# Optimization experiments

Measured on AMD Instinct MI355X. Metric: run time of the kernel, lower is better.

Reference implementation:

```python
import jax, jax.numpy as jnp
import numpy as np

B, N, D = 4, 4096, 1024
H, HD = 16, 64            # num_heads, head_dim (dim // num_heads)
K_ANCHOR = 256
SCALE = 1.0 / np.sqrt(float(HD))


def setup_inputs() -> dict:
    key = jax.random.key(0)
    ks = jax.random.split(key, 12)
    init = lambda k, shape, fan_in: jax.random.normal(k, shape, jnp.float32) * (1.0 / np.sqrt(fan_in))
    return {
        "x": jax.random.normal(ks[0], (B, N, D), jnp.float32),
        "Wq": init(ks[1], (D, H * HD), D), "bq": jnp.zeros((H * HD,), jnp.float32),
        "Wk": init(ks[2], (D, H * HD), D), "bk": jnp.zeros((H * HD,), jnp.float32),
        "Wv": init(ks[3], (D, H * HD), D), "bv": jnp.zeros((H * HD,), jnp.float32),
        "Wqt": init(ks[4], (D, D), D),     "bqt": jnp.zeros((D,), jnp.float32),
        "Wo": init(ks[5], (H * HD, D), H * HD), "bo": jnp.zeros((D,), jnp.float32),
        "num_anchor_tokens": K_ANCHOR,
    }


def _split_heads(t):
    # [B, S, H*HD] -> [B, H, S, HD]
    b, s, _ = t.shape
    return t.reshape(b, s, H, HD).transpose(0, 2, 1, 3)


def reference(x, Wq, bq, Wk, bk, Wv, bv, Wqt, bqt, Wo, bo, num_anchor_tokens):
    K = num_anchor_tokens  # static python int
    anchors = x[:, :K]     # [B, K, D]
    queries = x[:, K:]     # [B, N-K, D]

    q_a = anchors @ Wq + bq           # [B, K, H*HD]
    k_a = anchors @ Wk + bk           # [B, K, H*HD]
    v_a = anchors @ Wv + bv           # [B, K, H*HD]
    q_q = queries @ Wqt + bqt         # [B, N-K, H*HD] (dim == H*HD)

    q = _split_heads(jnp.concatenate([q_a, q_q], axis=1))  # [B, H, N, HD]
    k = _split_heads(k_a)                                  # [B, H, K, HD]
    v = _split_heads(v_a)                                  # [B, H, K, HD]

    scores = jnp.einsum("bhnd,bhkd->bhnk", q, k) * SCALE   # [B, H, N, K]
    weights = jax.nn.softmax(scores, axis=-1)
    ctx = jnp.einsum("bhnk,bhkd->bhnd", weights, v)        # [B, H, N, HD]
    ctx = ctx.transpose(0, 2, 1, 3).reshape(x.shape[0], x.shape[1], H * HD)
    return ctx @ Wo + bo               # [B, N, D]
```

## Files before the change

### kernel.cpp

```cpp
#include <hip/hip_runtime.h>
#include <stdint.h>
#include <stddef.h>


typedef _Float16 v8hf __attribute__((ext_vector_type(8)));
typedef _Float16 h4   __attribute__((ext_vector_type(4)));
typedef float    f32x4 __attribute__((ext_vector_type(4)));
typedef uint32_t u32x4 __attribute__((ext_vector_type(4)));

#define ATT_SCALE 0.125f
#define LOG2E     1.44269504088896340736f
#define QK_CE     (ATT_SCALE * LOG2E)

__device__ __forceinline__ void async16(const void* g, void* l) {
  __builtin_amdgcn_global_load_lds(
      (const __attribute__((address_space(1))) void*)g,
      (__attribute__((address_space(3))) void*)l,
      16, 0, 0);
}

__device__ __forceinline__ uint32_t pk_h2(float a, float b) {
  auto w = __builtin_amdgcn_cvt_pkrtz(a, b);
  return __builtin_bit_cast(uint32_t, w);
}

__global__ __launch_bounds__(256) void cvt_kernel(const float* __restrict__ src,
                                                  _Float16* __restrict__ dst, int n) {
  int i = (blockIdx.x * 256 + threadIdx.x) * 4;
  if (i + 3 < n) {
    float4 v = *(const float4*)(src + i);
    h4 o; o[0] = (_Float16)v.x; o[1] = (_Float16)v.y; o[2] = (_Float16)v.z; o[3] = (_Float16)v.w;
    *(h4*)(dst + i) = o;
  }
}

struct TPArgs { const float* src[5]; _Float16* dst[5]; };

__global__ __launch_bounds__(256) void transpose5_k(TPArgs a) {
  __shared__ _Float16 t[32][33];
  const int z = blockIdx.z;
  const float* __restrict__ src = a.src[z];
  _Float16* __restrict__ dst = a.dst[z];
  const int bx = blockIdx.x * 32, by = blockIdx.y * 32;
  const int x = threadIdx.x;
  for (int yy = threadIdx.y; yy < 32; yy += 8)
    t[yy][x] = (_Float16)src[(size_t)(by + yy) * 1024 + bx + x];
  __syncthreads();
  for (int yy = threadIdx.y; yy < 32; yy += 8)
    dst[(size_t)(bx + yy) * 1024 + by + x] = t[x][yy];
}

template <typename OutT>
__global__ __launch_bounds__(512, 2) void gemm256(
    const _Float16* __restrict__ A, const _Float16* __restrict__ Bt,
    const float* __restrict__ bias, OutT* __restrict__ out,
    int rowsPerBatch, int rowStart, float oscale)
{
  __shared__ __attribute__((aligned(16))) _Float16 As[4 * 256 * 32];
  __shared__ __attribute__((aligned(16))) _Float16 Bs[4 * 256 * 32];

  const int tid  = threadIdx.x;
  const int wave = tid >> 6, lane = tid & 63;
  const int quad = lane >> 4, l16 = lane & 15;
  const int wr = wave >> 2, wc = wave & 3;

  const int nwg = gridDim.x * gridDim.y;
  const int lin = blockIdx.y * 4 + blockIdx.x;
  const int swz = (lin & 7) * (nwg >> 3) + (lin >> 3);
  const int bx = swz & 3, by = swz >> 2;

  const int lrow = lane >> 2, lblk = lane & 3;

  auto gRowOf = [&](int m) -> int {
    int b = m / rowsPerBatch;
    return b * 4096 + rowStart + (m - b * rowsPerBatch);
  };

  const int tr0 = wave * 16 + lrow;
  const int tr1 = 128 + tr0;
  const _Float16* aS0 = A  + (size_t)gRowOf(by * 256 + tr0) * 1024 + (lblk ^ ((tr0 >> 1) & 3)) * 8;
  const _Float16* aS1 = A  + (size_t)gRowOf(by * 256 + tr1) * 1024 + (lblk ^ ((tr1 >> 1) & 3)) * 8;
  const _Float16* bS0 = Bt + (size_t)(bx * 256 + tr0) * 1024 + (lblk ^ ((tr0 >> 1) & 3)) * 8;
  const _Float16* bS1 = Bt + (size_t)(bx * 256 + tr1) * 1024 + (lblk ^ ((tr1 >> 1) & 3)) * 8;

  auto stage = [&](int t) {
    const int k0 = t * 32;
    _Float16* ad = As + (t & 3) * 8192 + wave * 512;
    _Float16* bd = Bs + (t & 3) * 8192 + wave * 512;
    async16(aS0 + k0, ad);
    async16(aS1 + k0, ad + 4096);
    async16(bS0 + k0, bd);
    async16(bS1 + k0, bd + 4096);
  };

  const int fblk = (quad ^ ((l16 >> 1) & 3)) * 8;

  f32x4 acc[8][4];
  #pragma unroll
  for (int i = 0; i < 8; i++)
    #pragma unroll
    for (int j = 0; j < 4; j++)
      acc[i][j] = f32x4{0.f, 0.f, 0.f, 0.f};

  stage(0); stage(1); stage(2);

  #pragma unroll 1
  for (int t = 0; t < 32; ++t) {
    if (t < 30)       asm volatile("s_waitcnt vmcnt(8)" ::: "memory");
    else if (t == 30) asm volatile("s_waitcnt vmcnt(4)" ::: "memory");
    else              asm volatile("s_waitcnt vmcnt(0)" ::: "memory");
    __builtin_amdgcn_s_barrier();
    __builtin_amdgcn_sched_barrier(0);
    asm volatile("" ::: "memory");

    if (t + 3 < 32) stage(t + 3);

    const _Float16* Ab = As + (t & 3) * 8192;
    const _Float16* Bb = Bs + (t & 3) * 8192;
    v8hf af[8], bf[4];
    #pragma unroll
    for (int nt = 0; nt < 4; nt++)
      bf[nt] = *(const v8hf*)(Bb + (wc * 64 + nt * 16 + l16) * 32 + fblk);
    #pragma unroll
    for (int mt = 0; mt < 8; mt++)
      af[mt] = *(const v8hf*)(Ab + (wr * 128 + mt * 16 + l16) * 32 + fblk);

    __builtin_amdgcn_s_setprio(1);
    #pragma unroll
    for (int mt = 0; mt < 8; mt++)
      #pragma unroll
      for (int nt = 0; nt < 4; nt++)
        acc[mt][nt] = __builtin_amdgcn_mfma_f32_16x16x32_f16(af[mt], bf[nt], acc[mt][nt], 0, 0, 0);
    __builtin_amdgcn_s_setprio(0);
  }

  const int colBase = bx * 256 + wc * 64;
  const int rowBase = by * 256 + wr * 128;
  #pragma unroll
  for (int mt = 0; mt < 8; mt++) {
    #pragma unroll
    for (int r = 0; r < 4; r++) {
      int m = rowBase + mt * 16 + quad * 4 + r;
      int b = m / rowsPerBatch;
      int rr = m - b * rowsPerBatch;
      #pragma unroll
      for (int nt = 0; nt < 4; nt++) {
        int col = colBase + nt * 16 + l16;
        float v = (acc[mt][nt][r] + bias[col]) * oscale;
        out[(size_t)(b * 4096 + rowStart + rr) * 1024 + col] = (OutT)v;
      }
    }
  }
}

template <typename OutT>
__global__ __launch_bounds__(256) void gemm64(
    const _Float16* __restrict__ A, const _Float16* __restrict__ Bt,
    const float* __restrict__ bias0, const float* __restrict__ bias1,
    const float* __restrict__ bias2,
    OutT* __restrict__ out0, _Float16* __restrict__ out1, _Float16* __restrict__ out2,
    int rowsPerBatch, int rowStart, int mode)
{
  __shared__ __attribute__((aligned(16))) _Float16 As[64 * 32];
  __shared__ __attribute__((aligned(16))) _Float16 Bs[128 * 32];

  const int tid  = threadIdx.x;
  const int wave = tid >> 6, lane = tid & 63;
  const int quad = lane >> 4, l16 = lane & 15;
  const int wr = wave >> 1, wc = wave & 1;

  const int gx = gridDim.x;
  const int lin = blockIdx.y * gx + blockIdx.x;
  const int x8 = lin & 7, j = lin >> 3;
  const int bx = j % gx;
  const int by = x8 * (gridDim.y >> 3) + j / gx;

  const int srow = lane >> 2;
  const int skol = (((lane & 3) ^ ((lane >> 3) & 3)) * 8);

  auto gRowOf = [&](int m) -> int {
    int b = m / rowsPerBatch;
    int r = m - b * rowsPerBatch;
    return b * 4096 + rowStart + r;
  };

  const int bc0 = wave * 2, bc1 = bc0 + 1;
  const _Float16* aS  = A  + (size_t)gRowOf(by * 64 + wave * 16 + srow) * 1024 + skol;
  const _Float16* bS0 = Bt + (size_t)(bx * 128 + bc0 * 16 + srow) * 1024 + skol;
  const _Float16* bS1 = Bt + (size_t)(bx * 128 + bc1 * 16 + srow) * 1024 + skol;
  _Float16* aD  = As + wave * 512;
  _Float16* bD0 = Bs + bc0 * 512;
  _Float16* bD1 = Bs + bc1 * 512;

  const int fblk = (quad ^ ((l16 >> 1) & 3)) * 8;

  f32x4 acc[2][4];
  #pragma unroll
  for (int i = 0; i < 2; i++)
    #pragma unroll
    for (int jj = 0; jj < 4; jj++)
      acc[i][jj] = f32x4{0.f, 0.f, 0.f, 0.f};

  for (int k0 = 0; k0 < 1024; k0 += 32) {
    __syncthreads();
    async16(aS  + k0, aD);
    async16(bS0 + k0, bD0);
    async16(bS1 + k0, bD1);
    __syncthreads();

    v8hf af[2], bfr[4];
    #pragma unroll
    for (int mt = 0; mt < 2; mt++)
      af[mt] = *(const v8hf*)(As + (wr * 32 + mt * 16 + l16) * 32 + fblk);
    #pragma unroll
    for (int nt = 0; nt < 4; nt++)
      bfr[nt] = *(const v8hf*)(Bs + (wc * 64 + nt * 16 + l16) * 32 + fblk);
    #pragma unroll
    for (int mt = 0; mt < 2; mt++)
      #pragma unroll
      for (int nt = 0; nt < 4; nt++)
        acc[mt][nt] = __builtin_amdgcn_mfma_f32_16x16x32_f16(af[mt], bfr[nt], acc[mt][nt], 0, 0, 0);
  }

  const int colBase = bx * 128 + wc * 64;
  const int rowBase = by * 64 + wr * 32;
  #pragma unroll
  for (int mt = 0; mt < 2; mt++) {
    #pragma unroll
    for (int r = 0; r < 4; r++) {
      int m = rowBase + mt * 16 + quad * 4 + r;
      int b = m / rowsPerBatch;
      int rr = m - b * rowsPerBatch;
      #pragma unroll
      for (int nt = 0; nt < 4; nt++) {
        int col = colBase + nt * 16 + l16;
        float v = acc[mt][nt][r];
        if (mode == 0) {
          v += bias0[col];
          out0[(size_t)(b * 4096 + rowStart + rr) * 1024 + col] = (OutT)v;
        } else {
          if (col < 1024) {
            v = (v + bias0[col]) * QK_CE;
            out0[(size_t)(b * 4096 + rr) * 1024 + col] = (OutT)v;
          } else if (col < 2048) {
            int c2 = col - 1024;
            v += bias1[c2];
            out1[(size_t)(b * 256 + rr) * 1024 + c2] = (_Float16)v;
          } else {
            int c2 = col - 2048;
            v += bias2[c2];
            int hh = c2 >> 6, d = c2 & 63;
            int kk = ((rr >> 7) & 1) * 128 + (rr & 15) * 8 + ((rr >> 4) & 7);
            int idx = ((kk >> 5) * 4 + (d >> 4)) * 512
                    + (((kk >> 3) & 3) * 16 + (d & 15)) * 8 + (kk & 7);
            out2[(size_t)(b * 16 + hh) * 16384 + idx] = (_Float16)v;
          }
        }
      }
    }
  }
}

__global__ __launch_bounds__(256, 5) void attn_kernel(
    const _Float16* __restrict__ q, const _Float16* __restrict__ k,
    const _Float16* __restrict__ vt, _Float16* __restrict__ ctx)
{
  __shared__ __attribute__((aligned(16))) _Float16 KP[256 * 64];

  const int tid  = threadIdx.x;
  const int wave = tid >> 6, lane = tid & 63;
  const int quad = lane >> 4, l16 = lane & 15;
  const int bid = blockIdx.x;
  const int qt = bid & 63, h = (bid >> 6) & 15, b = bid >> 10;

  const int fq = (l16 ^ (l16 >> 1)) & 7;

  const _Float16* kbase = k + (size_t)b * 256 * 1024 + h * 64;
  {
    const int s = lane >> 3;
    const int p = lane & 7;
    #pragma unroll
    for (int i = 0; i < 8; i++) {
      int c = wave * 8 + i;
      int row = c * 8 + s;
      int f = (row ^ (row >> 1)) & 7;
      async16(kbase + (size_t)row * 1024 + (p ^ f) * 8, KP + c * 512);
    }
  }

  const int qrow = qt * 64 + wave * 16 + l16;
  const _Float16* qbase = q + (size_t)(b * 4096 + qrow) * 1024 + h * 64 + quad * 8;
  v8hf a0 = *(const v8hf*)(qbase);
  v8hf a1 = *(const v8hf*)(qbase + 32);

  f32x4 s[16];
  #pragma unroll
  for (int t = 0; t < 16; t++) s[t] = f32x4{0.f, 0.f, 0.f, 0.f};

  __syncthreads();

  #pragma unroll
  for (int t = 0; t < 16; t++) {
    const _Float16* rbase = KP + (t * 16 + l16) * 64;
    int pb0 = (quad ^ fq) * 8;
    v8hf b0 = *(const v8hf*)(rbase + pb0);
    v8hf b1 = *(const v8hf*)(rbase + (pb0 ^ 32));
    s[t] = __builtin_amdgcn_mfma_f32_16x16x32_f16(a0, b0, s[t], 0, 0, 0);
    s[t] = __builtin_amdgcn_mfma_f32_16x16x32_f16(a1, b1, s[t], 0, 0, 0);
  }

  float inv[4];
  #pragma unroll
  for (int r = 0; r < 4; r++) {
    float m01 = fmaxf(s[0][r], s[1][r]),   m23 = fmaxf(s[2][r], s[3][r]);
    float m45 = fmaxf(s[4][r], s[5][r]),   m67 = fmaxf(s[6][r], s[7][r]);
    float m89 = fmaxf(s[8][r], s[9][r]),   mab = fmaxf(s[10][r], s[11][r]);
    float mcd = fmaxf(s[12][r], s[13][r]), mef = fmaxf(s[14][r], s[15][r]);
    float m = fmaxf(fmaxf(fmaxf(m01, m23), fmaxf(m45, m67)),
                    fmaxf(fmaxf(m89, mab), fmaxf(mcd, mef)));
    m = fmaxf(m, __shfl_xor(m, 1));
    m = fmaxf(m, __shfl_xor(m, 2));
    m = fmaxf(m, __shfl_xor(m, 4));
    m = fmaxf(m, __shfl_xor(m, 8));
    float sum = 0.f;
    #pragma unroll
    for (int t = 0; t < 16; t++) {
      float e = exp2f(s[t][r] - m);
      s[t][r] = e;
      sum += e;
    }
    sum += __shfl_xor(sum, 1);
    sum += __shfl_xor(sum, 2);
    sum += __shfl_xor(sum, 4);
    sum += __shfl_xor(sum, 8);
    inv[r] = 1.0f / sum;
  }

  __syncthreads();

  #pragma unroll
  for (int r = 0; r < 4; r++) {
    const int qr = quad * 4 + r;
    const int fp = (qr ^ (qr >> 1)) & 7;
    _Float16* prow = KP + (wave * 16 + qr) * 256;
    u32x4 lo, hi;
    #pragma unroll
    for (int j = 0; j < 4; j++) {
      lo[j] = pk_h2(s[2 * j][r],     s[2 * j + 1][r]);
      hi[j] = pk_h2(s[2 * j + 8][r], s[2 * j + 9][r]);
    }
    *(u32x4*)(prow + (l16 ^ fp) * 8)        = lo;
    *(u32x4*)(prow + ((l16 ^ fp) + 16) * 8) = hi;
  }

  asm volatile("s_waitcnt lgkmcnt(0)" ::: "memory");
  __builtin_amdgcn_sched_barrier(0);

  const _Float16* vlane = vt + (size_t)(b * 16 + h) * 16384 + lane * 8;
  f32x4 o[4];
  #pragma unroll
  for (int nt = 0; nt < 4; nt++) o[nt] = f32x4{0.f, 0.f, 0.f, 0.f};
  #pragma unroll
  for (int c = 0; c < 8; c++) {
    v8hf pa = *(const v8hf*)(KP + (wave * 16 + l16) * 256 + ((c * 4 + quad) ^ fq) * 8);
    #pragma unroll
    for (int nt = 0; nt < 4; nt++) {
      v8hf vb = *(const v8hf*)(vlane + (c * 4 + nt) * 512);
      o[nt] = __builtin_amdgcn_mfma_f32_16x16x32_f16(pa, vb, o[nt], 0, 0, 0);
    }
  }

  _Float16* obase = ctx + (size_t)(b * 4096 + qt * 64 + wave * 16 + quad * 4) * 1024 + h * 64;
  #pragma unroll
  for (int nt = 0; nt < 4; nt++)
    #pragma unroll
    for (int r = 0; r < 4; r++)
      obase[(size_t)r * 1024 + nt * 16 + l16] = (_Float16)(o[nt][r] * inv[r]);
}

extern "C" void kernel_launch(void* const* d_in, const int* in_sizes, int n_in,
                              void* d_out, int out_size, void* d_ws, size_t ws_size,
                              hipStream_t stream)
{
  (void)in_sizes; (void)n_in; (void)out_size; (void)ws_size;

  const float* x   = (const float*)d_in[0];
  const float* Wq  = (const float*)d_in[1];
  const float* bq  = (const float*)d_in[2];
  const float* Wk  = (const float*)d_in[3];
  const float* bk  = (const float*)d_in[4];
  const float* Wv  = (const float*)d_in[5];
  const float* bv  = (const float*)d_in[6];
  const float* Wqt = (const float*)d_in[7];
  const float* bqt = (const float*)d_in[8];
  const float* Wo  = (const float*)d_in[9];
  const float* bo  = (const float*)d_in[10];

  char* ws = (char*)d_ws;
  _Float16* xh    = (_Float16*)(ws);
  _Float16* WtQKV = (_Float16*)(ws + (32ll << 20));
  _Float16* WtQT  = (_Float16*)(ws + (38ll << 20));
  _Float16* WtO   = (_Float16*)(ws + (40ll << 20));
  _Float16* qbuf  = (_Float16*)(ws + (42ll << 20));
  _Float16* kbuf  = (_Float16*)(ws + (74ll << 20));
  _Float16* vtb   = (_Float16*)(ws + (76ll << 20));
  _Float16* ctxb  = (_Float16*)(ws + (78ll << 20));
  float* outp = (float*)d_out;

  const int nx = 4 * 4096 * 1024;
  cvt_kernel<<<nx / 1024, 256, 0, stream>>>(x, xh, nx);

  TPArgs tpa;
  tpa.src[0] = Wq;  tpa.dst[0] = WtQKV;
  tpa.src[1] = Wk;  tpa.dst[1] = WtQKV + 1024 * 1024;
  tpa.src[2] = Wv;  tpa.dst[2] = WtQKV + 2 * 1024 * 1024;
  tpa.src[3] = Wqt; tpa.dst[3] = WtQT;
  tpa.src[4] = Wo;  tpa.dst[4] = WtO;
  transpose5_k<<<dim3(32, 32, 5), dim3(32, 8), 0, stream>>>(tpa);

  gemm64<_Float16><<<dim3(24, 16), 256, 0, stream>>>(xh, WtQKV, bq, bk, bv,
                                                     qbuf, kbuf, vtb, 256, 0, 1);
  gemm256<_Float16><<<dim3(4, 60), 512, 0, stream>>>(xh, WtQT, bqt,
                                                     qbuf, 3840, 256, QK_CE);
  attn_kernel<<<4096, 256, 0, stream>>>(qbuf, kbuf, vtb, ctxb);
  gemm256<float><<<dim3(4, 64), 512, 0, stream>>>(ctxb, WtO, bo,
                                                  outp, 4096, 0, 1.0f);
}
```

Measured before the change: 310.0 us.

## Split GEMM K-step into two half-phases interleaving LDS reads, async stages and MFMA

Restructures the main GEMM loop so each K-step runs in two phases. Each phase loads half of the A fragments plus the B fragments from LDS, issues either the A or the B global-to-LDS async stage for step t+3, then runs 16 MFMAs, with barriers between phases in a ping-pong style schedule. The aim is to overlap global loads and LDS reads with matrix-core work and to hold fewer A fragment registers at once. In exchange it adds two to three extra barriers per iteration, which costs synchronisation overhead, and the reworked vmcnt waits must still match the number of loads in flight.

```diff
diff --git a/kernel.cpp b/kernel.cpp
--- a/kernel.cpp
+++ b/kernel.cpp
@@ -83,12 +83,15 @@
   const _Float16* bS0 = Bt + (size_t)(bx * 256 + tr0) * 1024 + (lblk ^ ((tr0 >> 1) & 3)) * 8;
   const _Float16* bS1 = Bt + (size_t)(bx * 256 + tr1) * 1024 + (lblk ^ ((tr1 >> 1) & 3)) * 8;
 
-  auto stage = [&](int t) {
+  auto stageA = [&](int t) {
     const int k0 = t * 32;
     _Float16* ad = As + (t & 3) * 8192 + wave * 512;
-    _Float16* bd = Bs + (t & 3) * 8192 + wave * 512;
     async16(aS0 + k0, ad);
     async16(aS1 + k0, ad + 4096);
+  };
+  auto stageB = [&](int t) {
+    const int k0 = t * 32;
+    _Float16* bd = Bs + (t & 3) * 8192 + wave * 512;
     async16(bS0 + k0, bd);
     async16(bS1 + k0, bd + 4096);
   };
@@ -102,36 +105,53 @@
     for (int j = 0; j < 4; j++)
       acc[i][j] = f32x4{0.f, 0.f, 0.f, 0.f};
 
-  stage(0); stage(1); stage(2);
+  stageA(0); stageB(0); stageA(1); stageB(1); stageA(2); stageB(2);
+  asm volatile("s_waitcnt vmcnt(8)" ::: "memory");
+  __builtin_amdgcn_s_barrier();
 
   #pragma unroll 1
   for (int t = 0; t < 32; ++t) {
-    if (t < 30)       asm volatile("s_waitcnt vmcnt(8)" ::: "memory");
-    else if (t == 30) asm volatile("s_waitcnt vmcnt(4)" ::: "memory");
+    const _Float16* Ab = As + (t & 3) * 8192;
+    const _Float16* Bb = Bs + (t & 3) * 8192;
+    v8hf af0[4], af1[4], bf[4];
+
+    #pragma unroll
+    for (int nt = 0; nt < 4; nt++)
+      bf[nt] = *(const v8hf*)(Bb + (wc * 64 + nt * 16 + l16) * 32 + fblk);
+    #pragma unroll
+    for (int mt = 0; mt < 4; mt++)
+      af0[mt] = *(const v8hf*)(Ab + (wr * 128 + mt * 16 + l16) * 32 + fblk);
+    if (t + 3 < 32) stageA(t + 3);
+    __builtin_amdgcn_s_barrier();
+    asm volatile("s_waitcnt lgkmcnt(0)" ::: "memory");
+    __builtin_amdgcn_sched_barrier(0);
+    __builtin_amdgcn_s_setprio(1);
+    #pragma unroll
+    for (int mt = 0; mt < 4; mt++)
+      #pragma unroll
+      for (int nt = 0; nt < 4; nt++)
+        acc[mt][nt] = __builtin_amdgcn_mfma_f32_16x16x32_f16(af0[mt], bf[nt], acc[mt][nt], 0, 0, 0);
+    __builtin_amdgcn_s_setprio(0);
+    __builtin_amdgcn_s_barrier();
+
+    #pragma unroll
+    for (int mt = 0; mt < 4; mt++)
+      af1[mt] = *(const v8hf*)(Ab + (wr * 128 + (mt + 4) * 16 + l16) * 32 + fblk);
+    if (t + 3 < 32) stageB(t + 3);
+    if (t <= 28)      asm volatile("s_waitcnt vmcnt(6)" ::: "memory");
+    else if (t == 29) asm volatile("s_waitcnt vmcnt(4)" ::: "memory");
     else              asm volatile("s_waitcnt vmcnt(0)" ::: "memory");
     __builtin_amdgcn_s_barrier();
+    asm volatile("s_waitcnt lgkmcnt(0)" ::: "memory");
     __builtin_amdgcn_sched_barrier(0);
-    asm volatile("" ::: "memory");
-
-    if (t + 3 < 32) stage(t + 3);
-
-    const _Float16* Ab = As + (t & 3) * 8192;
-    const _Float16* Bb = Bs + (t & 3) * 8192;
-    v8hf af[8], bf[4];
-    #pragma unroll
-    for (int nt = 0; nt < 4; nt++)
-      bf[nt] = *(const v8hf*)(Bb + (wc * 64 + nt * 16 + l16) * 32 + fblk);
-    #pragma unroll
-    for (int mt = 0; mt < 8; mt++)
-      af[mt] = *(const v8hf*)(Ab + (wr * 128 + mt * 16 + l16) * 32 + fblk);
-
     __builtin_amdgcn_s_setprio(1);
     #pragma unroll
-    for (int mt = 0; mt < 8; mt++)
+    for (int mt = 0; mt < 4; mt++)
       #pragma unroll
       for (int nt = 0; nt < 4; nt++)
-        acc[mt][nt] = __builtin_amdgcn_mfma_f32_16x16x32_f16(af[mt], bf[nt], acc[mt][nt], 0, 0, 0);
+        acc[mt + 4][nt] = __builtin_amdgcn_mfma_f32_16x16x32_f16(af1[mt], bf[nt], acc[mt + 4][nt], 0, 0, 0);
     __builtin_amdgcn_s_setprio(0);
+    __builtin_amdgcn_s_barrier();
   }
 
   const int colBase = bx * 256 + wc * 64;
```

Result: no change. 306.8 us (-1.0%).
